# Kernel tuning notes

Hardware: AMD Instinct MI355X
Metric: run time of the kernel (lower is better)

Reference implementation:

```python
import jax, jax.numpy as jnp
import numpy as np

N_NODES = 50000
N_EDGES = 800000
IN_CH = 64
HID_CH = 64
OUT_CH = 64
NUM_GRAPHS = 256


def setup_inputs() -> dict:
    key = jax.random.key(0)
    ks = jax.random.split(key, 9)
    x = jax.random.normal(ks[0], (N_NODES, IN_CH), dtype=jnp.float32)
    edge_index = jax.random.randint(ks[1], (2, N_EDGES), 0, N_NODES, dtype=jnp.int64)
    batch = jnp.sort(jax.random.randint(ks[2], (N_NODES,), 0, NUM_GRAPHS, dtype=jnp.int64))
    def glorot(k, fan_in, fan_out):
        s = jnp.sqrt(6.0 / (fan_in + fan_out))
        return jax.random.uniform(k, (fan_in, fan_out), jnp.float32, -s, s)
    W1 = glorot(ks[3], IN_CH, HID_CH)
    b1 = jnp.zeros((HID_CH,), jnp.float32)
    W2 = glorot(ks[4], HID_CH, HID_CH)
    b2 = jnp.zeros((HID_CH,), jnp.float32)
    W3 = glorot(ks[5], HID_CH, OUT_CH)
    b3 = jnp.zeros((OUT_CH,), jnp.float32)
    return {"x": x, "edge_index": edge_index, "batch": batch,
            "W1": W1, "b1": b1, "W2": W2, "b2": b2, "W3": W3, "b3": b3}


def gcn_conv(x, src, dst, W, b):
    # PyG GCNConv: linear, add self-loops, symmetric deg normalization, scatter-add, bias
    n = x.shape[0]
    xw = x @ W                                   # [N, F_out]
    loops = jnp.arange(n, dtype=src.dtype)
    s = jnp.concatenate([src, loops])            # sources (with self loops)
    d = jnp.concatenate([dst, loops])            # targets (with self loops)
    ones = jnp.ones(d.shape, dtype=x.dtype)
    deg = jax.ops.segment_sum(ones, d, num_segments=n)
    dinv = jnp.where(deg > 0, jax.lax.rsqrt(deg), 0.0)
    norm = dinv[s] * dinv[d]                     # [E + N]
    msgs = norm[:, None] * xw[s]                 # gather + scale
    out = jax.ops.segment_sum(msgs, d, num_segments=n)
    return out + b


def reference(x, edge_index, batch, W1, b1, W2, b2, W3, b3):
    src, dst = edge_index[0], edge_index[1]
    h = jax.nn.relu(gcn_conv(x, src, dst, W1, b1))
    h = jax.nn.relu(gcn_conv(h, src, dst, W2, b2))
    h = gcn_conv(h, src, dst, W3, b3)
    # global_add_pool over graph ids
    pooled = jax.ops.segment_sum(h, batch, num_segments=NUM_GRAPHS)  # [G, OUT_CH]
    return pooled  # out_channels != 1, so no flatten
```

## Files before the change

### kernel.cpp

```cpp
#include <hip/hip_runtime.h>
#include <hip/hip_bf16.h>
#include <hip/hip_fp16.h>

#define N_NODES 50000
#define N_EDGES 800000
#define CH 64
#define N_GRAPHS 256
#define NBUCK 196
#define CHUNK 4096
#define NHIST 98

__device__ __forceinline__ unsigned bf16_rne(float f) {
    unsigned u = __float_as_uint(f);
    return (u + 0x7fffu + ((u >> 16) & 1u)) >> 16;
}
__device__ __forceinline__ float4 ldtab(const unsigned short* __restrict__ tab, int s, int c4) {
    uint2 u = *(const uint2*)(tab + ((size_t)s << 6) + c4);
    float4 r;
    r.x = __uint_as_float(u.x << 16);
    r.y = __uint_as_float(u.x & 0xffff0000u);
    r.z = __uint_as_float(u.y << 16);
    r.w = __uint_as_float(u.y & 0xffff0000u);
    return r;
}
__device__ __forceinline__ unsigned pack_sn(int s, float n) {
    return (unsigned)s | ((unsigned)__half_as_ushort(__float2half_rn(n)) << 16);
}
__device__ __forceinline__ float unpack_n(unsigned p) {
    return __half2float(__ushort_as_half((unsigned short)(p >> 16)));
}

__global__ void edge_hist(const int* __restrict__ ei, int* __restrict__ hpart) {
    __shared__ int h[NBUCK];
    for (int i = threadIdx.x; i < NBUCK; i += 256) h[i] = 0;
    __syncthreads();
    int t = blockIdx.x * 256 + threadIdx.x;
    int stride = NHIST * 256 * 4;
    for (int e = t * 4; e < N_EDGES; e += stride) {
        int4 d = *(const int4*)&ei[N_EDGES + e];
        atomicAdd(&h[d.x >> 8], 1);
        atomicAdd(&h[d.y >> 8], 1);
        atomicAdd(&h[d.z >> 8], 1);
        atomicAdd(&h[d.w >> 8], 1);
    }
    __syncthreads();
    for (int i = threadIdx.x; i < NBUCK; i += 256)
        hpart[blockIdx.x * NBUCK + i] = h[i];
}

__global__ void bucket_scan(const int* __restrict__ hpart, int* __restrict__ bstart,
                            int* __restrict__ gcur, float* __restrict__ poolz) {
    int i = blockIdx.x * 256 + threadIdx.x;
    if (i < N_GRAPHS * CH + N_GRAPHS) poolz[i] = 0.0f;
    if (blockIdx.x != 0) return;
    __shared__ int sc[256];
    int tid = threadIdx.x;
    int v = 0;
    if (tid < NBUCK)
        for (int r = 0; r < NHIST; ++r) v += hpart[r * NBUCK + tid];
    sc[tid] = v;
    __syncthreads();
    for (int off = 1; off < 256; off <<= 1) {
        int t = (tid >= off) ? sc[tid - off] : 0;
        __syncthreads();
        sc[tid] += t;
        __syncthreads();
    }
    if (tid < NBUCK) {
        int ex = sc[tid] - v;
        bstart[tid] = ex;
        gcur[tid] = ex;
    }
    if (tid == 255) bstart[NBUCK] = sc[255];
}

__global__ __launch_bounds__(512) void bin_scatter(const int* __restrict__ ei,
                                                   int* __restrict__ gcur,
                                                   unsigned* __restrict__ ebuf) {
    __shared__ int hist[NBUCK];
    __shared__ int lofs[NBUCK];
    __shared__ int gbase[NBUCK];
    __shared__ int cur[NBUCK];
    __shared__ int sc[512];
    __shared__ unsigned stage[CHUNK];
    int tid = threadIdx.x;
    for (int i = tid; i < NBUCK; i += 512) hist[i] = 0;
    __syncthreads();
    int e0 = blockIdx.x * CHUNK;
    int n = min(CHUNK, N_EDGES - e0);
    int src[8], dst[8];
#pragma unroll
    for (int k = 0; k < 8; ++k) {
        int idx = k * 512 + tid;
        if (idx < n) {
            int e = e0 + idx;
            src[k] = ei[e];
            dst[k] = ei[N_EDGES + e];
            atomicAdd(&hist[dst[k] >> 8], 1);
        } else dst[k] = -1;
    }
    __syncthreads();
    int v = (tid < NBUCK) ? hist[tid] : 0;
    sc[tid] = v;
    __syncthreads();
    for (int off = 1; off < 512; off <<= 1) {
        int t = (tid >= off) ? sc[tid - off] : 0;
        __syncthreads();
        sc[tid] += t;
        __syncthreads();
    }
    if (tid < NBUCK) {
        int ex = sc[tid] - v;
        lofs[tid] = ex;
        cur[tid] = ex;
        gbase[tid] = v ? atomicAdd(&gcur[tid], v) : 0;
    }
    __syncthreads();
#pragma unroll
    for (int k = 0; k < 8; ++k) {
        if (dst[k] >= 0) {
            int b = dst[k] >> 8;
            int p = atomicAdd(&cur[b], 1);
            stage[p] = (unsigned)src[k] | ((unsigned)(dst[k] & 255) << 16)
                                        | ((unsigned)b << 24);
        }
    }
    __syncthreads();
    for (int i = tid; i < n; i += 512) {
        unsigned p = stage[i];
        int b = p >> 24;
        ebuf[gbase[b] + (i - lofs[b])] = p;
    }
}

__global__ void csr_bucket(const unsigned* __restrict__ ebuf, const int* __restrict__ bstart,
                           int* __restrict__ deg, int* __restrict__ rowp,
                           float* __restrict__ dinv, int* __restrict__ col) {
    __shared__ int nd[256];
    __shared__ int cur[256];
    __shared__ int sc[256];
    int b = blockIdx.x;
    int tid = threadIdx.x;
    nd[tid] = 0;
    __syncthreads();
    int es = bstart[b], ee = bstart[b + 1];
    for (int e = es + tid; e < ee; e += 256)
        atomicAdd(&nd[(ebuf[e] >> 16) & 255], 1);
    __syncthreads();
    int v = nd[tid];
    sc[tid] = v;
    __syncthreads();
    for (int off = 1; off < 256; off <<= 1) {
        int t = (tid >= off) ? sc[tid - off] : 0;
        __syncthreads();
        sc[tid] += t;
        __syncthreads();
    }
    int node = b * 256 + tid;
    int lstart = es + sc[tid] - v;
    if (node < N_NODES) {
        deg[node] = v;
        rowp[node] = lstart;
        dinv[node] = rsqrtf((float)v + 1.0f);
    }
    cur[tid] = lstart;
    __syncthreads();
    for (int e = es + tid; e < ee; e += 256) {
        unsigned p = ebuf[e];
        int pos = atomicAdd(&cur[(p >> 16) & 255], 1);
        col[pos] = (int)(p & 0xFFFFu);
    }
}

__global__ void gemm_reg(const float* __restrict__ in, const float* __restrict__ W,
                         unsigned short* __restrict__ out, int n) {
    __shared__ float WT[64 * 68];
    int tid = threadIdx.x;
    for (int i = tid; i < 64 * 64; i += 256) {
        int k = i >> 6, c = i & 63;
        WT[c * 68 + k] = W[i];
    }
    __syncthreads();
    int lane = tid & 63;
    int wv = __builtin_amdgcn_readfirstlane(tid >> 6);
    int row0 = blockIdx.x * 32 + wv * 8;
    if (row0 >= n) return;
    float acc[8] = {0.f, 0.f, 0.f, 0.f, 0.f, 0.f, 0.f, 0.f};
#pragma unroll 2
    for (int k = 0; k < 64; k += 4) {
        float4 w = *(const float4*)&WT[lane * 68 + k];
#pragma unroll
        for (int r = 0; r < 8; ++r) {
            float4 xv = *(const float4*)&in[(size_t)(row0 + r) * 64 + k];
            acc[r] = fmaf(xv.x, w.x, acc[r]);
            acc[r] = fmaf(xv.y, w.y, acc[r]);
            acc[r] = fmaf(xv.z, w.z, acc[r]);
            acc[r] = fmaf(xv.w, w.w, acc[r]);
        }
    }
#pragma unroll
    for (int r = 0; r < 8; ++r)
        out[(size_t)(row0 + r) * 64 + lane] = (unsigned short)bf16_rne(acc[r]);
}

template <int OUT_BF16, int USE_PCK, int WRITE_PCK>
__global__ void agg_v4(const int* __restrict__ rowp, const int* __restrict__ deg,
                       const int* __restrict__ col, const float* __restrict__ dinv,
                       unsigned* __restrict__ pck,
                       const unsigned short* __restrict__ tab, const float* __restrict__ bias,
                       void* __restrict__ outv, int do_relu) {
    int wv = __builtin_amdgcn_readfirstlane(threadIdx.x >> 6);
    int node = blockIdx.x * 4 + wv;
    int lane = threadIdx.x & 63;
    int q = lane >> 4;
    int c4 = (lane & 15) << 2;
    float dd = dinv[node];
    int cnt = deg[node];
    int start = rowp[node];
    float4 acc = make_float4(0.f, 0.f, 0.f, 0.f);
    if (q == 0) {
        float4 xs = ldtab(tab, node, c4);
        float dd2 = dd * dd;
        acc.x = xs.x * dd2; acc.y = xs.y * dd2; acc.z = xs.z * dd2; acc.w = xs.w * dd2;
    }
    int j = 0;
    for (; j + 8 <= cnt; j += 8) {
        int sA, sB;
        float nA, nB;
        if (USE_PCK) {
            unsigned pA = pck[start + j + q];
            unsigned pB = pck[start + j + 4 + q];
            sA = (int)(pA & 0xFFFFu); nA = unpack_n(pA);
            sB = (int)(pB & 0xFFFFu); nB = unpack_n(pB);
        } else {
            sA = col[start + j + q];
            sB = col[start + j + 4 + q];
            nA = dinv[sA] * dd;
            nB = dinv[sB] * dd;
        }
        float4 xA = ldtab(tab, sA, c4);
        float4 xB = ldtab(tab, sB, c4);
        if (WRITE_PCK && (lane & 15) == 0) {
            pck[start + j + q] = pack_sn(sA, nA);
            pck[start + j + 4 + q] = pack_sn(sB, nB);
        }
        acc.x = fmaf(nA, xA.x, acc.x); acc.y = fmaf(nA, xA.y, acc.y);
        acc.z = fmaf(nA, xA.z, acc.z); acc.w = fmaf(nA, xA.w, acc.w);
        acc.x = fmaf(nB, xB.x, acc.x); acc.y = fmaf(nB, xB.y, acc.y);
        acc.z = fmaf(nB, xB.z, acc.z); acc.w = fmaf(nB, xB.w, acc.w);
    }
    for (; j < cnt; j += 4) {
        int jj = j + q;
        bool valid = jj < cnt;
        int s;
        float nv;
        if (USE_PCK) {
            unsigned p = pck[start + (valid ? jj : 0)];
            s = (int)(p & 0xFFFFu);
            nv = valid ? unpack_n(p) : 0.0f;
        } else {
            s = col[start + (valid ? jj : 0)];
            nv = valid ? dinv[s] * dd : 0.0f;
            if (WRITE_PCK && valid && (lane & 15) == 0)
                pck[start + jj] = pack_sn(s, nv);
        }
        float4 xv = ldtab(tab, s, c4);
        acc.x = fmaf(nv, xv.x, acc.x); acc.y = fmaf(nv, xv.y, acc.y);
        acc.z = fmaf(nv, xv.z, acc.z); acc.w = fmaf(nv, xv.w, acc.w);
    }
    acc.x += __shfl_xor(acc.x, 16); acc.y += __shfl_xor(acc.y, 16);
    acc.z += __shfl_xor(acc.z, 16); acc.w += __shfl_xor(acc.w, 16);
    acc.x += __shfl_xor(acc.x, 32); acc.y += __shfl_xor(acc.y, 32);
    acc.z += __shfl_xor(acc.z, 32); acc.w += __shfl_xor(acc.w, 32);
    if (q == 0) {
        if (bias) {
            float4 bv = *(const float4*)&bias[c4];
            acc.x += bv.x; acc.y += bv.y; acc.z += bv.z; acc.w += bv.w;
        }
        if (do_relu) {
            acc.x = fmaxf(acc.x, 0.f); acc.y = fmaxf(acc.y, 0.f);
            acc.z = fmaxf(acc.z, 0.f); acc.w = fmaxf(acc.w, 0.f);
        }
        if (OUT_BF16) {
            uint2 o;
            o.x = bf16_rne(acc.x) | (bf16_rne(acc.y) << 16);
            o.y = bf16_rne(acc.z) | (bf16_rne(acc.w) << 16);
            *(uint2*)&((unsigned short*)outv)[((size_t)node << 6) + c4] = o;
        } else {
            *(float4*)&((float*)outv)[((size_t)node << 6) + c4] = acc;
        }
    }
}

__global__ void pool_seg(const unsigned short* __restrict__ h, const int* __restrict__ batch,
                         float* __restrict__ pool, float* __restrict__ cntg) {
    int ch = threadIdx.x & 63;
    int grp = threadIdx.x >> 6;
    int base = (blockIdx.x * 4 + grp) * 16;
    float acc = 0.0f;
    int curg = -1, runlen = 0;
    for (int n = 0; n < 16; ++n) {
        int node = base + n;
        if (node >= N_NODES) break;
        int g = batch[node];
        float v = __uint_as_float(((unsigned)h[((size_t)node << 6) + ch]) << 16);
        if (g != curg) {
            if (curg >= 0) {
                atomicAdd(&pool[curg * 64 + ch], acc);
                if (ch == 0) atomicAdd(&cntg[curg], (float)runlen);
            }
            curg = g; acc = v; runlen = 1;
        } else { acc += v; runlen++; }
    }
    if (curg >= 0) {
        atomicAdd(&pool[curg * 64 + ch], acc);
        if (ch == 0) atomicAdd(&cntg[curg], (float)runlen);
    }
}

__global__ void out_gemm(const float* __restrict__ P, const float* __restrict__ cntg,
                         const float* __restrict__ W, const float* __restrict__ b,
                         float* __restrict__ out) {
    __shared__ float Ws[64 * 64];
    int tid = threadIdx.x;
    for (int i = tid; i < 64 * 64; i += 256) Ws[i] = W[i];
    __syncthreads();
    int lane = tid & 63;
    int g = blockIdx.x * 4 + (tid >> 6);
    if (g >= N_GRAPHS) return;
    float pv = P[g * 64 + lane];
    float acc = 0.0f;
#pragma unroll
    for (int k = 0; k < 64; ++k)
        acc = fmaf(__shfl(pv, k, 64), Ws[k * 64 + lane], acc);
    out[g * 64 + lane] = acc + cntg[g] * b[lane];
}

extern "C" void kernel_launch(void* const* d_in, const int* in_sizes, int n_in,
                              void* d_out, int out_size, void* d_ws, size_t ws_size,
                              hipStream_t stream) {
    const float* x   = (const float*)d_in[0];
    const int* ei    = (const int*)d_in[1];
    const int* batch = (const int*)d_in[2];
    const float* W1  = (const float*)d_in[3];
    const float* b1  = (const float*)d_in[4];
    const float* W2  = (const float*)d_in[5];
    const float* b2  = (const float*)d_in[6];
    const float* W3  = (const float*)d_in[7];
    const float* b3  = (const float*)d_in[8];
    float* out = (float*)d_out;

    char* ws = (char*)d_ws;
    float*    dinv  = (float*)(ws);
    int*      DEG   = (int*)(ws + 200192);
    int*      ROWP  = (int*)(ws + 400384);
    int*      COL   = (int*)(ws + 600576);
    unsigned* PCK   = (unsigned*)(ws + 3800576);
    int*      HPART = (int*)(ws + 7000576);
    int*      BST   = (int*)(ws + 7077888);
    int*      GCUR  = (int*)(ws + 7078912);
    float*    XW    = (float*)(ws + 7080960);
    unsigned* EBUF  = (unsigned*)(ws + 7080960);
    float*    ACC   = (float*)(ws + 19880960);
    float*    POOL  = (float*)(ws + 32680960);
    float*    CNT   = (float*)(ws + 32746496);

    const int WAVE_NODE_BLK = N_NODES / 4;
    const int GEMM_BLK = (N_NODES + 31) / 32;
    const int SCAT_BLK = (N_EDGES + CHUNK - 1) / CHUNK;

    edge_hist<<<NHIST, 256, 0, stream>>>(ei, HPART);
    bucket_scan<<<65, 256, 0, stream>>>(HPART, BST, GCUR, POOL);
    bin_scatter<<<SCAT_BLK, 512, 0, stream>>>(ei, GCUR, EBUF);
    csr_bucket<<<NBUCK, 256, 0, stream>>>(EBUF, BST, DEG, ROWP, dinv, COL);

    gemm_reg<<<GEMM_BLK, 256, 0, stream>>>(x, W1, (unsigned short*)XW, N_NODES);
    agg_v4<0, 0, 1><<<WAVE_NODE_BLK, 256, 0, stream>>>(ROWP, DEG, COL, dinv, PCK,
        (const unsigned short*)XW, b1, ACC, 1);

    gemm_reg<<<GEMM_BLK, 256, 0, stream>>>(ACC, W2, (unsigned short*)XW, N_NODES);
    agg_v4<1, 1, 0><<<WAVE_NODE_BLK, 256, 0, stream>>>(ROWP, DEG, COL, dinv, PCK,
        (const unsigned short*)XW, b2, ACC, 1);

    agg_v4<1, 1, 0><<<WAVE_NODE_BLK, 256, 0, stream>>>(ROWP, DEG, COL, dinv, PCK,
        (const unsigned short*)ACC, nullptr, XW, 0);
    pool_seg<<<(N_NODES + 63) / 64, 256, 0, stream>>>((const unsigned short*)XW,
        batch, POOL, CNT);
    out_gemm<<<N_GRAPHS / 4, 256, 0, stream>>>(POOL, CNT, W3, b3, out);
}
```

Before: 242.2 us.

## Store layer-1 output as bf16, unroll gathers by four, shrink scatter blocks

The first aggregation now writes bf16 instead of fp32, and the second GEMM reads bf16 input. This halves the write and read traffic for that intermediate. The aggregation loop loads four packed index/norm words before the four row gathers, which raises memory-level parallelism. The bin_scatter kernel moves to 256-thread blocks over 2048-edge chunks, so it launches more, smaller blocks. The extra bf16 rounding of the hidden activations slightly changes the numerics.

```diff
diff --git a/kernel.cpp b/kernel.cpp
--- a/kernel.cpp
+++ b/kernel.cpp
@@ -7,7 +7,7 @@
 #define CH 64
 #define N_GRAPHS 256
 #define NBUCK 196
-#define CHUNK 4096
+#define CHUNK 2048
 #define NHIST 98
 
 __device__ __forceinline__ unsigned bf16_rne(float f) {
@@ -74,24 +74,24 @@
     if (tid == 255) bstart[NBUCK] = sc[255];
 }
 
-__global__ __launch_bounds__(512) void bin_scatter(const int* __restrict__ ei,
+__global__ __launch_bounds__(256) void bin_scatter(const int* __restrict__ ei,
                                                    int* __restrict__ gcur,
                                                    unsigned* __restrict__ ebuf) {
     __shared__ int hist[NBUCK];
     __shared__ int lofs[NBUCK];
     __shared__ int gbase[NBUCK];
     __shared__ int cur[NBUCK];
-    __shared__ int sc[512];
+    __shared__ int sc[256];
     __shared__ unsigned stage[CHUNK];
     int tid = threadIdx.x;
-    for (int i = tid; i < NBUCK; i += 512) hist[i] = 0;
+    for (int i = tid; i < NBUCK; i += 256) hist[i] = 0;
     __syncthreads();
     int e0 = blockIdx.x * CHUNK;
     int n = min(CHUNK, N_EDGES - e0);
     int src[8], dst[8];
 #pragma unroll
     for (int k = 0; k < 8; ++k) {
-        int idx = k * 512 + tid;
+        int idx = k * 256 + tid;
         if (idx < n) {
             int e = e0 + idx;
             src[k] = ei[e];
@@ -103,7 +103,7 @@
     int v = (tid < NBUCK) ? hist[tid] : 0;
     sc[tid] = v;
     __syncthreads();
-    for (int off = 1; off < 512; off <<= 1) {
+    for (int off = 1; off < 256; off <<= 1) {
         int t = (tid >= off) ? sc[tid - off] : 0;
         __syncthreads();
         sc[tid] += t;
@@ -126,7 +126,7 @@
         }
     }
     __syncthreads();
-    for (int i = tid; i < n; i += 512) {
+    for (int i = tid; i < n; i += 256) {
         unsigned p = stage[i];
         int b = p >> 24;
         ebuf[gbase[b] + (i - lofs[b])] = p;
@@ -172,7 +172,8 @@
     }
 }
 
-__global__ void gemm_reg(const float* __restrict__ in, const float* __restrict__ W,
+template <int IN_BF16>
+__global__ void gemm_reg(const void* __restrict__ inv, const float* __restrict__ W,
                          unsigned short* __restrict__ out, int n) {
     __shared__ float WT[64 * 68];
     int tid = threadIdx.x;
@@ -186,16 +187,38 @@
     int row0 = blockIdx.x * 32 + wv * 8;
     if (row0 >= n) return;
     float acc[8] = {0.f, 0.f, 0.f, 0.f, 0.f, 0.f, 0.f, 0.f};
+    if (IN_BF16) {
+        const unsigned short* in = (const unsigned short*)inv;
 #pragma unroll 2
-    for (int k = 0; k < 64; k += 4) {
-        float4 w = *(const float4*)&WT[lane * 68 + k];
-#pragma unroll
-        for (int r = 0; r < 8; ++r) {
-            float4 xv = *(const float4*)&in[(size_t)(row0 + r) * 64 + k];
-            acc[r] = fmaf(xv.x, w.x, acc[r]);
-            acc[r] = fmaf(xv.y, w.y, acc[r]);
-            acc[r] = fmaf(xv.z, w.z, acc[r]);
-            acc[r] = fmaf(xv.w, w.w, acc[r]);
+        for (int k = 0; k < 64; k += 8) {
+            float4 w0 = *(const float4*)&WT[lane * 68 + k];
+            float4 w1 = *(const float4*)&WT[lane * 68 + k + 4];
+#pragma unroll
+            for (int r = 0; r < 8; ++r) {
+                uint4 xb = *(const uint4*)&in[(size_t)(row0 + r) * 64 + k];
+                acc[r] = fmaf(__uint_as_float(xb.x << 16),         w0.x, acc[r]);
+                acc[r] = fmaf(__uint_as_float(xb.x & 0xffff0000u), w0.y, acc[r]);
+                acc[r] = fmaf(__uint_as_float(xb.y << 16),         w0.z, acc[r]);
+                acc[r] = fmaf(__uint_as_float(xb.y & 0xffff0000u), w0.w, acc[r]);
+                acc[r] = fmaf(__uint_as_float(xb.z << 16),         w1.x, acc[r]);
+                acc[r] = fmaf(__uint_as_float(xb.z & 0xffff0000u), w1.y, acc[r]);
+                acc[r] = fmaf(__uint_as_float(xb.w << 16),         w1.z, acc[r]);
+                acc[r] = fmaf(__uint_as_float(xb.w & 0xffff0000u), w1.w, acc[r]);
+            }
+        }
+    } else {
+        const float* in = (const float*)inv;
+#pragma unroll 2
+        for (int k = 0; k < 64; k += 4) {
+            float4 w = *(const float4*)&WT[lane * 68 + k];
+#pragma unroll
+            for (int r = 0; r < 8; ++r) {
+                float4 xv = *(const float4*)&in[(size_t)(row0 + r) * 64 + k];
+                acc[r] = fmaf(xv.x, w.x, acc[r]);
+                acc[r] = fmaf(xv.y, w.y, acc[r]);
+                acc[r] = fmaf(xv.z, w.z, acc[r]);
+                acc[r] = fmaf(xv.w, w.w, acc[r]);
+            }
         }
     }
 #pragma unroll
@@ -224,36 +247,54 @@
         acc.x = xs.x * dd2; acc.y = xs.y * dd2; acc.z = xs.z * dd2; acc.w = xs.w * dd2;
     }
     int j = 0;
+    for (; j + 16 <= cnt; j += 16) {
+        int s[4]; float nv[4];
+#pragma unroll
+        for (int u = 0; u < 4; ++u) {
+            int idx = start + j + 4 * u + q;
+            if (USE_PCK) {
+                unsigned p = pck[idx];
+                s[u] = (int)(p & 0xFFFFu);
+                nv[u] = unpack_n(p);
+            } else {
+                s[u] = col[idx];
+                nv[u] = dinv[s[u]] * dd;
+                if (WRITE_PCK && (lane & 15) == 0) pck[idx] = pack_sn(s[u], nv[u]);
+            }
+        }
+#pragma unroll
+        for (int u = 0; u < 4; ++u) {
+            float4 xv = ldtab(tab, s[u], c4);
+            acc.x = fmaf(nv[u], xv.x, acc.x); acc.y = fmaf(nv[u], xv.y, acc.y);
+            acc.z = fmaf(nv[u], xv.z, acc.z); acc.w = fmaf(nv[u], xv.w, acc.w);
+        }
+    }
     for (; j + 8 <= cnt; j += 8) {
-        int sA, sB;
-        float nA, nB;
-        if (USE_PCK) {
-            unsigned pA = pck[start + j + q];
-            unsigned pB = pck[start + j + 4 + q];
-            sA = (int)(pA & 0xFFFFu); nA = unpack_n(pA);
-            sB = (int)(pB & 0xFFFFu); nB = unpack_n(pB);
-        } else {
-            sA = col[start + j + q];
-            sB = col[start + j + 4 + q];
-            nA = dinv[sA] * dd;
-            nB = dinv[sB] * dd;
-        }
-        float4 xA = ldtab(tab, sA, c4);
-        float4 xB = ldtab(tab, sB, c4);
-        if (WRITE_PCK && (lane & 15) == 0) {
-            pck[start + j + q] = pack_sn(sA, nA);
-            pck[start + j + 4 + q] = pack_sn(sB, nB);
-        }
-        acc.x = fmaf(nA, xA.x, acc.x); acc.y = fmaf(nA, xA.y, acc.y);
-        acc.z = fmaf(nA, xA.z, acc.z); acc.w = fmaf(nA, xA.w, acc.w);
-        acc.x = fmaf(nB, xB.x, acc.x); acc.y = fmaf(nB, xB.y, acc.y);
-        acc.z = fmaf(nB, xB.z, acc.z); acc.w = fmaf(nB, xB.w, acc.w);
+        int s[2]; float nv[2];
+#pragma unroll
+        for (int u = 0; u < 2; ++u) {
+            int idx = start + j + 4 * u + q;
+            if (USE_PCK) {
+                unsigned p = pck[idx];
+                s[u] = (int)(p & 0xFFFFu);
+                nv[u] = unpack_n(p);
+            } else {
+                s[u] = col[idx];
+                nv[u] = dinv[s[u]] * dd;
+                if (WRITE_PCK && (lane & 15) == 0) pck[idx] = pack_sn(s[u], nv[u]);
+            }
+        }
+#pragma unroll
+        for (int u = 0; u < 2; ++u) {
+            float4 xv = ldtab(tab, s[u], c4);
+            acc.x = fmaf(nv[u], xv.x, acc.x); acc.y = fmaf(nv[u], xv.y, acc.y);
+            acc.z = fmaf(nv[u], xv.z, acc.z); acc.w = fmaf(nv[u], xv.w, acc.w);
+        }
     }
     for (; j < cnt; j += 4) {
         int jj = j + q;
         bool valid = jj < cnt;
-        int s;
-        float nv;
+        int s; float nv;
         if (USE_PCK) {
             unsigned p = pck[start + (valid ? jj : 0)];
             s = (int)(p & 0xFFFFu);
@@ -261,8 +302,7 @@
         } else {
             s = col[start + (valid ? jj : 0)];
             nv = valid ? dinv[s] * dd : 0.0f;
-            if (WRITE_PCK && valid && (lane & 15) == 0)
-                pck[start + jj] = pack_sn(s, nv);
+            if (WRITE_PCK && valid && (lane & 15) == 0) pck[start + jj] = pack_sn(s, nv);
         }
         float4 xv = ldtab(tab, s, c4);
         acc.x = fmaf(nv, xv.x, acc.x); acc.y = fmaf(nv, xv.y, acc.y);
@@ -371,14 +411,14 @@
 
     edge_hist<<<NHIST, 256, 0, stream>>>(ei, HPART);
     bucket_scan<<<65, 256, 0, stream>>>(HPART, BST, GCUR, POOL);
-    bin_scatter<<<SCAT_BLK, 512, 0, stream>>>(ei, GCUR, EBUF);
+    bin_scatter<<<SCAT_BLK, 256, 0, stream>>>(ei, GCUR, EBUF);
     csr_bucket<<<NBUCK, 256, 0, stream>>>(EBUF, BST, DEG, ROWP, dinv, COL);
 
-    gemm_reg<<<GEMM_BLK, 256, 0, stream>>>(x, W1, (unsigned short*)XW, N_NODES);
-    agg_v4<0, 0, 1><<<WAVE_NODE_BLK, 256, 0, stream>>>(ROWP, DEG, COL, dinv, PCK,
+    gemm_reg<0><<<GEMM_BLK, 256, 0, stream>>>(x, W1, (unsigned short*)XW, N_NODES);
+    agg_v4<1, 0, 1><<<WAVE_NODE_BLK, 256, 0, stream>>>(ROWP, DEG, COL, dinv, PCK,
         (const unsigned short*)XW, b1, ACC, 1);
 
-    gemm_reg<<<GEMM_BLK, 256, 0, stream>>>(ACC, W2, (unsigned short*)XW, N_NODES);
+    gemm_reg<1><<<GEMM_BLK, 256, 0, stream>>>(ACC, W2, (unsigned short*)XW, N_NODES);
     agg_v4<1, 1, 0><<<WAVE_NODE_BLK, 256, 0, stream>>>(ROWP, DEG, COL, dinv, PCK,
         (const unsigned short*)XW, b2, ACC, 1);
 
```

Result: no change. 244.3 us (+0.9%).
